# Optimization experiments

Hardware: AMD Instinct MI355X
Metric: run time of the kernel (lower is better)

## Reference

```python
import jax, jax.numpy as jnp
import numpy as np
from jax import lax

NUM_CLASSES = 10
NUM_ITER = 3
DN = ('NCHW', 'OIHW', 'NCHW')


def squash(t, axis=-1):
    sq = (t ** 2).sum(axis=axis, keepdims=True)
    return (sq / (1.0 + sq)) * t / jnp.sqrt(sq)


def setup_inputs() -> dict:
    key = jax.random.key(0)
    ks = jax.random.split(key, 12)
    B = 512
    s = 0.05  # param scale for numerical stability
    return {
        'x': jax.random.normal(ks[0], (B, 1, 28, 28), jnp.float32),
        'conv1_w': jax.random.normal(ks[1], (256, 1, 9, 9), jnp.float32) * s,
        'conv1_b': jax.random.normal(ks[2], (256,), jnp.float32) * s,
        'prim_w': jax.random.normal(ks[3], (8, 32, 256, 9, 9), jnp.float32) * s,
        'prim_b': jax.random.normal(ks[4], (8, 32), jnp.float32) * s,
        'route_w': jax.random.normal(ks[5], (NUM_CLASSES, 32 * 6 * 6, 8, 16), jnp.float32),
        'dec_w1': jax.random.normal(ks[6], (512, 16 * NUM_CLASSES), jnp.float32) * s,
        'dec_b1': jax.random.normal(ks[7], (512,), jnp.float32) * s,
        'dec_w2': jax.random.normal(ks[8], (1024, 512), jnp.float32) * s,
        'dec_b2': jax.random.normal(ks[9], (1024,), jnp.float32) * s,
        'dec_w3': jax.random.normal(ks[10], (784, 1024), jnp.float32) * s,
        'dec_b3': jax.random.normal(ks[11], (784,), jnp.float32) * s,
    }


def reference(x, conv1_w, conv1_b, prim_w, prim_b, route_w,
              dec_w1, dec_b1, dec_w2, dec_b2, dec_w3, dec_b3):
    B = x.shape[0]
    # conv1 + relu: [B,256,20,20]
    h = lax.conv_general_dilated(x, conv1_w, (1, 1), 'VALID', dimension_numbers=DN)
    h = jax.nn.relu(h + conv1_b[None, :, None, None])
    # primary capsules: 8 parallel convs fused into one conv with 8*32 out channels
    kw = prim_w.reshape(8 * 32, 256, 9, 9)
    u = lax.conv_general_dilated(h, kw, (2, 2), 'VALID', dimension_numbers=DN)
    u = u + prim_b.reshape(-1)[None, :, None, None]          # [B,256,6,6]
    u = u.reshape(B, 8, 32 * 6 * 6).transpose(0, 2, 1)       # [B,1152,8]
    u = squash(u, axis=-1)
    # digit capsules: priors [C,B,R,16]
    priors = jnp.einsum('bri,crio->cbro', u, route_w)
    logits = jnp.zeros_like(priors)
    for i in range(NUM_ITER):
        probs = jax.nn.softmax(logits, axis=2)
        v = squash((probs * priors).sum(axis=2, keepdims=True))  # [C,B,1,16]
        if i != NUM_ITER - 1:
            logits = logits + (priors * v).sum(axis=-1, keepdims=True)
    caps = v.squeeze(2).transpose(1, 0, 2)                    # [B,C,16]
    classes = jnp.sqrt((caps ** 2).sum(axis=-1))              # [B,C]
    classes = jax.nn.softmax(classes, axis=1)
    y = jax.nn.one_hot(jnp.argmax(classes, axis=1), NUM_CLASSES, dtype=caps.dtype)
    d = (caps * y[:, :, None]).reshape(B, -1)                 # [B,160]
    d = jax.nn.relu(d @ dec_w1.T + dec_b1)
    d = jax.nn.relu(d @ dec_w2.T + dec_b2)
    recon = jax.nn.sigmoid(d @ dec_w3.T + dec_b3)             # [B,784]
    return classes, recon
```

## Files before the change

kernel.cpp:

```cpp
#include <hip/hip_runtime.h>
#include <math.h>


typedef _Float16 f16;
typedef _Float16 f16x8 __attribute__((ext_vector_type(8)));
typedef _Float16 f16x4 __attribute__((ext_vector_type(4)));
typedef float f32x4 __attribute__((ext_vector_type(4)));

__device__ __forceinline__ void gl_lds16(const void* g, void* l) {
  __builtin_amdgcn_global_load_lds(
      (const __attribute__((address_space(1))) void*)g,
      (__attribute__((address_space(3))) void*)l, 16, 0, 0);
}

__global__ __launch_bounds__(256, 2) void conv1_kernel(
    const float* __restrict__ x, const float* __restrict__ w,
    const float* __restrict__ bias, f16* __restrict__ ht)
{
  __shared__ float xs[784];
  const int b = blockIdx.x;
  const int t = threadIdx.x;
  for (int i = t; i < 784; i += 256) xs[i] = x[b * 784 + i];
  float wr[81];
#pragma unroll
  for (int k = 0; k < 81; ++k) wr[k] = w[t * 81 + k];
  const float bv = bias[t];
  __syncthreads();
  for (int oy = 0; oy < 20; ++oy) {
    float acc[20];
#pragma unroll
    for (int i = 0; i < 20; ++i) acc[i] = bv;
#pragma unroll
    for (int ky = 0; ky < 9; ++ky) {
      float xr[28];
#pragma unroll
      for (int q = 0; q < 7; ++q) {
        const float4 v = *(const float4*)&xs[(oy + ky) * 28 + q * 4];
        xr[q*4+0] = v.x; xr[q*4+1] = v.y; xr[q*4+2] = v.z; xr[q*4+3] = v.w;
      }
#pragma unroll
      for (int kx = 0; kx < 9; ++kx) {
        const float wv = wr[ky * 9 + kx];
#pragma unroll
        for (int ox = 0; ox < 20; ++ox) acc[ox] = fmaf(xr[ox + kx], wv, acc[ox]);
      }
    }
    f16* hp = &ht[(size_t)((b * 20 + oy) * 20) * 256 + t];
#pragma unroll
    for (int ox = 0; ox < 20; ++ox)
      hp[ox * 256] = (f16)fmaxf(acc[ox], 0.f);
  }
}

__global__ __launch_bounds__(256) void wtrans_kernel(
    const float* __restrict__ w, f16* __restrict__ wt)
{
  __shared__ float tile[64 * 83];
  const int oc = blockIdx.x;
  const int icq = blockIdx.y;
  const int t = threadIdx.x;
  const float* src = w + (size_t)oc * 20736 + (size_t)icq * 64 * 81;
  for (int idx = t; idx < 5184; idx += 256) {
    const int ici = idx / 81, kk = idx - ici * 81;
    tile[ici * 83 + kk] = src[idx];
  }
  __syncthreads();
  f16* dst = wt + (size_t)oc * 20736 + icq * 64;
  for (int idx = t; idx < 5184; idx += 256) {
    const int kk = idx >> 6, ici = idx & 63;
    dst[kk * 256 + ici] = (f16)tile[ici * 83 + kk];
  }
}

__global__ __launch_bounds__(256) void prim_mfma_kernel(
    const f16* __restrict__ ht, const f16* __restrict__ wt,
    float* __restrict__ part)
{
  __shared__ f16 sm[10240];
  f16* As = sm;
  f16* Bs = sm + 2048;
  const int t = threadIdx.x;
  const int wv = t >> 6, lane = t & 63;
  const int id = blockIdx.x;
  const int ks = (id & 7) >> 1;
  const int mb = ((id >> 3) << 1) | (id & 1);
  const int m0 = mb * 64;

  const int chunk = (lane & 3) ^ ((lane >> 3) & 3);
  long aoff;
  {
    const int r = wv * 16 + (lane >> 2);
    const int m = m0 + r;
    const int b = m / 36, pos = m - b * 36;
    const int oy = pos / 6, ox = pos - oy * 6;
    aoff = (long)(((b * 20 + 2 * oy) * 20 + 2 * ox) * 256) * 2 + chunk * 16;
  }
  long boff[4];
#pragma unroll
  for (int i = 0; i < 4; ++i) {
    const int r = i * 64 + wv * 16 + (lane >> 2);
    boff[i] = (long)r * 41472 + chunk * 16;
  }
  const char* htc = (const char*)ht;
  const char* wtc = (const char*)wt;

  const int lrow = lane & 15, quad = lane >> 4;
  const int qx = quad ^ ((lrow >> 1) & 3);
  f32x4 acc[4][4] = {};

  const int s0 = ks * 162, s1 = s0 + 162;
  for (int s = s0; s < s1; ++s) {
    const int kykx = s >> 3, icb = s & 7;
    const int ky = kykx / 9, kx = kykx - ky * 9;
    const long astep = (long)((((ky * 20 + kx) * 256) + icb * 32) * 2);
    const long bstep = (long)(((kykx * 256) + icb * 32) * 2);
    __syncthreads();
    {
      gl_lds16(htc + aoff + astep, (char*)As + wv * 1024);
#pragma unroll
      for (int i = 0; i < 4; ++i)
        gl_lds16(wtc + boff[i] + bstep, (char*)Bs + i * 4096 + wv * 1024);
    }
    __syncthreads();
    f16x8 af[4], bf[4];
#pragma unroll
    for (int mt = 0; mt < 4; ++mt)
      af[mt] = *(const f16x8*)&As[(mt * 16 + lrow) * 32 + qx * 8];
#pragma unroll
    for (int nt = 0; nt < 4; ++nt)
      bf[nt] = *(const f16x8*)&Bs[(wv * 64 + nt * 16 + lrow) * 32 + qx * 8];
#pragma unroll
    for (int mt = 0; mt < 4; ++mt)
#pragma unroll
      for (int nt = 0; nt < 4; ++nt)
        acc[mt][nt] = __builtin_amdgcn_mfma_f32_16x16x32_f16(
            af[mt], bf[nt], acc[mt][nt], 0, 0, 0);
  }

  float* pp = part + (size_t)ks * 4718592;
#pragma unroll
  for (int mt = 0; mt < 4; ++mt) {
    const int mbase = m0 + mt * 16 + quad * 4;
#pragma unroll
    for (int nt = 0; nt < 4; ++nt) {
      const int n = wv * 64 + nt * 16 + lrow;
      const int np = (n & 31) * 8 + (n >> 5);
#pragma unroll
      for (int rg = 0; rg < 4; ++rg)
        pp[(size_t)(mbase + rg) * 256 + np] = acc[mt][nt][rg];
    }
  }
}

__global__ void squash_kernel(const float* __restrict__ part,
                              const float* __restrict__ bias,
                              float* __restrict__ u)
{
  const int tid = blockIdx.x * 256 + threadIdx.x;
  if (tid >= 512 * 36 * 32) return;
  const int cc = tid & 31;
  const int row = tid >> 5;
  const int b = row / 36;
  const int pos = row - b * 36;
  const float* p = part + (size_t)row * 256 + cc * 8;
  float v[8] = {};
#pragma unroll
  for (int ksl = 0; ksl < 4; ++ksl) {
    const float4 a0 = *(const float4*)(p + (size_t)ksl * 4718592);
    const float4 a1 = *(const float4*)(p + (size_t)ksl * 4718592 + 4);
    v[0] += a0.x; v[1] += a0.y; v[2] += a0.z; v[3] += a0.w;
    v[4] += a1.x; v[5] += a1.y; v[6] += a1.z; v[7] += a1.w;
  }
  float sq = 0.f;
#pragma unroll
  for (int i = 0; i < 8; ++i) {
    v[i] += bias[i * 32 + cc];
    sq = fmaf(v[i], v[i], sq);
  }
  const float scale = sq / ((1.f + sq) * sqrtf(sq));
  float* up = &u[(size_t)(b * 1152 + cc * 36 + pos) * 8];
#pragma unroll
  for (int i = 0; i < 8; ++i) up[i] = v[i] * scale;
}

__global__ __launch_bounds__(256, 4) void priors_kernel(
    const float* __restrict__ u, const float* __restrict__ rw,
    f16* __restrict__ P)
{
  const int t = threadIdx.x;
  const int rl = t >> 2, oq = t & 3;
  const int r = blockIdx.x * 64 + rl;
  const int b0 = blockIdx.y * 64;
  const int c = blockIdx.z;

  float4 wreg[8];
  const float* wbase = rw + (size_t)(c * 1152 + r) * 128 + oq * 4;
#pragma unroll
  for (int k = 0; k < 8; ++k)
    wreg[k] = *(const float4*)(wbase + k * 16);

  f16* pbase = P + (size_t)((c * 512 + b0) * 1152 + r) * 16 + oq * 4;
  const float* ubase = u + (size_t)(b0 * 1152 + r) * 8;

  for (int b = 0; b < 64; ++b) {
    const float4 ua = *(const float4*)(ubase + (size_t)b * 9216);
    const float4 ub = *(const float4*)(ubase + (size_t)b * 9216 + 4);
    const float uu[8] = {ua.x, ua.y, ua.z, ua.w, ub.x, ub.y, ub.z, ub.w};
    float ax = 0.f, ay = 0.f, az = 0.f, aw = 0.f;
#pragma unroll
    for (int k = 0; k < 8; ++k) {
      ax = fmaf(uu[k], wreg[k].x, ax);
      ay = fmaf(uu[k], wreg[k].y, ay);
      az = fmaf(uu[k], wreg[k].z, az);
      aw = fmaf(uu[k], wreg[k].w, aw);
    }
    f16x4 st;
    st[0] = (f16)ax; st[1] = (f16)ay; st[2] = (f16)az; st[3] = (f16)aw;
    *(f16x4*)(pbase + (size_t)b * 18432) = st;
  }
}

__device__ __forceinline__ float wave_sum(float v) {
#pragma unroll
  for (int off = 32; off > 0; off >>= 1) v += __shfl_xor(v, off);
  return v;
}
__device__ __forceinline__ float wave_max(float v) {
#pragma unroll
  for (int off = 32; off > 0; off >>= 1) v = fmaxf(v, __shfl_xor(v, off));
  return v;
}

__global__ __launch_bounds__(256, 2) void routing_kernel(
    const f16* __restrict__ Pg, float* __restrict__ caps)
{
  const int c = blockIdx.x >> 9;
  const int b = blockIdx.x & 511;
  const int t = threadIdx.x;
  const int wid = t >> 6;
  const int lane = t & 63;
  __shared__ float xred[4 * 17];

  float P[5][16];
  float lg[5];
  const int nk = (t < 128) ? 5 : 4;
#pragma unroll
  for (int k = 0; k < 5; ++k)
#pragma unroll
    for (int o = 0; o < 16; ++o) P[k][o] = 0.f;

  const f16* pbase = Pg + (size_t)((c * 512 + b) * 1152) * 16;
#pragma unroll
  for (int k = 0; k < 5; ++k) {
    if (k < nk) {
      const int r = t + (k << 8);
      const f16x8 p0 = *(const f16x8*)&pbase[(size_t)r * 16];
      const f16x8 p1 = *(const f16x8*)&pbase[(size_t)r * 16 + 8];
#pragma unroll
      for (int o = 0; o < 8; ++o) {
        P[k][o]     = (float)p0[o];
        P[k][o + 8] = (float)p1[o];
      }
    }
  }

  float v[16];
  {
    float sq = 0.f;
#pragma unroll
    for (int o = 0; o < 16; ++o) {
      float p = 0.f;
#pragma unroll
      for (int k = 0; k < 5; ++k) p += P[k][o];
      p = wave_sum(p);
      if (lane == 0) xred[wid * 17 + o] = p;
      v[o] = 0.f;
    }
    __syncthreads();
#pragma unroll
    for (int o = 0; o < 16; ++o) {
      const float s = (xred[o] + xred[17 + o] + xred[34 + o] + xred[51 + o]) *
                      (1.f / 1152.f);
      v[o] = s;
      sq = fmaf(s, s, sq);
    }
    const float scale = sq / ((1.f + sq) * sqrtf(sq));
#pragma unroll
    for (int o = 0; o < 16; ++o) v[o] *= scale;
    __syncthreads();
  }
#pragma unroll
  for (int k = 0; k < 5; ++k) {
    float a = 0.f;
#pragma unroll
    for (int o = 0; o < 16; ++o) a = fmaf(P[k][o], v[o], a);
    lg[k] = a;
  }

  for (int it = 1; it < 3; ++it) {
    float m = -1e30f;
#pragma unroll
    for (int k = 0; k < 5; ++k) if (k < nk) m = fmaxf(m, lg[k]);
    m = wave_max(m);
    if (lane == 0) xred[wid * 17 + 16] = m;
    __syncthreads();
    const float mx = fmaxf(fmaxf(xred[16], xred[17 + 16]),
                           fmaxf(xred[34 + 16], xred[51 + 16]));
    __syncthreads();
    float e[5];
#pragma unroll
    for (int k = 0; k < 5; ++k) e[k] = (k < nk) ? expf(lg[k] - mx) : 0.f;
    float pS = 0.f;
#pragma unroll
    for (int k = 0; k < 5; ++k) pS += e[k];
    pS = wave_sum(pS);
    if (lane == 0) xred[wid * 17 + 16] = pS;
#pragma unroll
    for (int o = 0; o < 16; ++o) {
      float p = 0.f;
#pragma unroll
      for (int k = 0; k < 5; ++k) p = fmaf(e[k], P[k][o], p);
      p = wave_sum(p);
      if (lane == 0) xred[wid * 17 + o] = p;
    }
    __syncthreads();
    const float S = xred[16] + xred[17 + 16] + xred[34 + 16] + xred[51 + 16];
    const float inv = 1.f / S;
    float sq = 0.f;
#pragma unroll
    for (int o = 0; o < 16; ++o) {
      const float s = (xred[o] + xred[17 + o] + xred[34 + o] + xred[51 + o]) * inv;
      v[o] = s;
      sq = fmaf(s, s, sq);
    }
    const float scale = sq / ((1.f + sq) * sqrtf(sq));
#pragma unroll
    for (int o = 0; o < 16; ++o) v[o] *= scale;
    __syncthreads();
    if (it < 2) {
#pragma unroll
      for (int k = 0; k < 5; ++k) {
        float a = 0.f;
#pragma unroll
        for (int o = 0; o < 16; ++o) a = fmaf(P[k][o], v[o], a);
        lg[k] += a;
      }
    }
  }
  if (t == 0) {
    float* cp = &caps[(b * 10 + c) * 16];
#pragma unroll
    for (int o = 0; o < 16; ++o) cp[o] = v[o];
  }
}

__global__ void classes_kernel(const float* __restrict__ caps,
                               float* __restrict__ out_classes,
                               float* __restrict__ d0)
{
  const int b = blockIdx.x * 256 + threadIdx.x;
  if (b >= 512) return;
  float nrm[10];
#pragma unroll
  for (int cc = 0; cc < 10; ++cc) {
    float sq = 0.f;
#pragma unroll
    for (int o = 0; o < 16; ++o) {
      const float vv = caps[(b * 10 + cc) * 16 + o];
      sq = fmaf(vv, vv, sq);
    }
    nrm[cc] = sqrtf(sq);
  }
  float mx = nrm[0]; int cs = 0;
#pragma unroll
  for (int cc = 1; cc < 10; ++cc)
    if (nrm[cc] > mx) { mx = nrm[cc]; cs = cc; }
  float e[10], ssum = 0.f;
#pragma unroll
  for (int cc = 0; cc < 10; ++cc) { e[cc] = expf(nrm[cc] - mx); ssum += e[cc]; }
  const float inv = 1.f / ssum;
#pragma unroll
  for (int cc = 0; cc < 10; ++cc) out_classes[b * 10 + cc] = e[cc] * inv;
#pragma unroll
  for (int cc = 0; cc < 10; ++cc)
#pragma unroll
    for (int o = 0; o < 16; ++o)
      d0[b * 160 + cc * 16 + o] = (cc == cs) ? caps[(b * 10 + cc) * 16 + o] : 0.f;
}

__global__ __launch_bounds__(256, 2) void fc_kernel(
    const float* __restrict__ A, const float* __restrict__ W,
    const float* __restrict__ bias, float* __restrict__ C,
    int N, int K, int act)
{
  __shared__ float As[64][17];
  __shared__ float Ws[64][17];
  const int t = threadIdx.x;
  const int tm = t >> 4, tn = t & 15;
  const int m0 = blockIdx.y << 6, n0 = blockIdx.x << 6;
  const int lr = t >> 2, lq = (t & 3) << 2;
  float acc[4][4] = {};
  for (int k0 = 0; k0 < K; k0 += 16) {
    const float4 av = *(const float4*)&A[(m0 + lr) * K + k0 + lq];
    float4 wv = make_float4(0.f, 0.f, 0.f, 0.f);
    const int wn = n0 + lr;
    if (wn < N) wv = *(const float4*)&W[wn * K + k0 + lq];
    __syncthreads();
    As[lr][lq+0] = av.x; As[lr][lq+1] = av.y; As[lr][lq+2] = av.z; As[lr][lq+3] = av.w;
    Ws[lr][lq+0] = wv.x; Ws[lr][lq+1] = wv.y; Ws[lr][lq+2] = wv.z; Ws[lr][lq+3] = wv.w;
    __syncthreads();
#pragma unroll
    for (int kk = 0; kk < 16; ++kk) {
      float a[4], w[4];
#pragma unroll
      for (int i = 0; i < 4; ++i) a[i] = As[tm * 4 + i][kk];
#pragma unroll
      for (int j = 0; j < 4; ++j) w[j] = Ws[tn * 4 + j][kk];
#pragma unroll
      for (int i = 0; i < 4; ++i)
#pragma unroll
        for (int j = 0; j < 4; ++j) acc[i][j] = fmaf(a[i], w[j], acc[i][j]);
    }
  }
#pragma unroll
  for (int i = 0; i < 4; ++i) {
    const int m = m0 + tm * 4 + i;
#pragma unroll
    for (int j = 0; j < 4; ++j) {
      const int n = n0 + tn * 4 + j;
      if (n < N) {
        float vv = acc[i][j] + bias[n];
        vv = act ? (1.f / (1.f + expf(-vv))) : fmaxf(vv, 0.f);
        C[m * N + n] = vv;
      }
    }
  }
}

extern "C" void kernel_launch(void* const* d_in, const int* in_sizes, int n_in,
                              void* d_out, int out_size, void* d_ws, size_t ws_size,
                              hipStream_t stream)
{
  const float* x       = (const float*)d_in[0];
  const float* conv1_w = (const float*)d_in[1];
  const float* conv1_b = (const float*)d_in[2];
  const float* prim_w  = (const float*)d_in[3];
  const float* prim_b  = (const float*)d_in[4];
  const float* route_w = (const float*)d_in[5];
  const float* dec_w1  = (const float*)d_in[6];
  const float* dec_b1  = (const float*)d_in[7];
  const float* dec_w2  = (const float*)d_in[8];
  const float* dec_b2  = (const float*)d_in[9];
  const float* dec_w3  = (const float*)d_in[10];
  const float* dec_b3  = (const float*)d_in[11];
  float* out = (float*)d_out;

  char* ws = (char*)d_ws;
  f16*   ht   = (f16*)(ws);
  f16*   wtp  = (f16*)(ws + 104857600);
  float* part = (float*)(ws + 115474432);
  float* u    = (float*)(ws + 190971904);
  f16*   P    = (f16*)(ws);
  float* caps = (float*)(ws + 209846272);
  float* d0   = (float*)(ws + 210173952);
  float* d1   = (float*)(ws + 210501632);
  float* d2   = (float*)(ws + 211550208);

  hipLaunchKernelGGL(conv1_kernel, dim3(512), dim3(256), 0, stream,
                     x, conv1_w, conv1_b, ht);
  hipLaunchKernelGGL(wtrans_kernel, dim3(256, 4), dim3(256), 0, stream,
                     prim_w, wtp);
  hipLaunchKernelGGL(prim_mfma_kernel, dim3(1152), dim3(256), 0, stream,
                     ht, wtp, part);
  hipLaunchKernelGGL(squash_kernel, dim3(2304), dim3(256), 0, stream,
                     part, prim_b, u);
  hipLaunchKernelGGL(priors_kernel, dim3(18, 8, 10), dim3(256), 0, stream,
                     u, route_w, P);
  hipLaunchKernelGGL(routing_kernel, dim3(5120), dim3(256), 0, stream,
                     P, caps);
  hipLaunchKernelGGL(classes_kernel, dim3(2), dim3(256), 0, stream,
                     caps, out, d0);
  hipLaunchKernelGGL(fc_kernel, dim3(8, 8), dim3(256), 0, stream,
                     d0, dec_w1, dec_b1, d1, 512, 160, 0);
  hipLaunchKernelGGL(fc_kernel, dim3(16, 8), dim3(256), 0, stream,
                     d1, dec_w2, dec_b2, d2, 1024, 512, 0);
  hipLaunchKernelGGL(fc_kernel, dim3(13, 8), dim3(256), 0, stream,
                     d2, dec_w3, dec_b3, out + 5120, 784, 1024, 1);
}
```

Before: 857.3 us.

## Retile primary-capsule MFMA GEMM to 128x128 blocks with 64-wide K steps

Changes the primary-capsule conv GEMM block tile from 64x256 with K=32 per step to 128x128 with K=64 per step, using a 2x2 wave layout and an 8-chunk XOR swizzle in LDS. Each barrier pair now covers two MFMA rounds, halving the number of K iterations and synchronisation points. The square tile balances global loads between A and B. LDS use grows to 32KB per block and the grid mapping is reorganised across M, N and K-split.

After: 841.5 us. About the same (-1.8%).

```diff
diff --git a/kernel.cpp b/kernel.cpp
--- a/kernel.cpp
+++ b/kernel.cpp
@@ -76,74 +76,80 @@
     const f16* __restrict__ ht, const f16* __restrict__ wt,
     float* __restrict__ part)
 {
-  __shared__ f16 sm[10240];
-  f16* As = sm;
-  f16* Bs = sm + 2048;
+  __shared__ f16 sm[16384];
   const int t = threadIdx.x;
   const int wv = t >> 6, lane = t & 63;
   const int id = blockIdx.x;
-  const int ks = (id & 7) >> 1;
-  const int mb = ((id >> 3) << 1) | (id & 1);
-  const int m0 = mb * 64;
-
-  const int chunk = (lane & 3) ^ ((lane >> 3) & 3);
-  long aoff;
-  {
-    const int r = wv * 16 + (lane >> 2);
+  const int g = id >> 3;
+  const int ks = g & 3;
+  const int nb = (g >> 2) & 1;
+  const int mb = (id & 7) + 8 * (g >> 3);
+  const int m0 = mb * 128, n0 = nb * 128;
+
+  const int chunk = (lane & 7) ^ ((lane >> 3) & 7);
+  long aoff[4], boff[4];
+#pragma unroll
+  for (int i = 0; i < 4; ++i) {
+    const int r = wv * 32 + i * 8 + (lane >> 3);
     const int m = m0 + r;
     const int b = m / 36, pos = m - b * 36;
     const int oy = pos / 6, ox = pos - oy * 6;
-    aoff = (long)(((b * 20 + 2 * oy) * 20 + 2 * ox) * 256) * 2 + chunk * 16;
-  }
-  long boff[4];
-#pragma unroll
-  for (int i = 0; i < 4; ++i) {
-    const int r = i * 64 + wv * 16 + (lane >> 2);
-    boff[i] = (long)r * 41472 + chunk * 16;
+    aoff[i] = (long)(((b * 20 + 2 * oy) * 20 + 2 * ox) * 256) * 2 + chunk * 16;
+    boff[i] = (long)(n0 + r) * 41472 + chunk * 16;
   }
   const char* htc = (const char*)ht;
   const char* wtc = (const char*)wt;
 
   const int lrow = lane & 15, quad = lane >> 4;
-  const int qx = quad ^ ((lrow >> 1) & 3);
+  const int wm = wv & 1, wn = wv >> 1;
   f32x4 acc[4][4] = {};
 
-  const int s0 = ks * 162, s1 = s0 + 162;
+  const int s0 = ks * 81, s1 = s0 + 81;
   for (int s = s0; s < s1; ++s) {
-    const int kykx = s >> 3, icb = s & 7;
+    const int kykx = s >> 2, icb = s & 3;
     const int ky = kykx / 9, kx = kykx - ky * 9;
-    const long astep = (long)((((ky * 20 + kx) * 256) + icb * 32) * 2);
-    const long bstep = (long)(((kykx * 256) + icb * 32) * 2);
+    const long astep = (long)((((ky * 20 + kx) * 256) + icb * 64) * 2);
+    const long bstep = (long)(((kykx * 256) + icb * 64) * 2);
     __syncthreads();
     {
-      gl_lds16(htc + aoff + astep, (char*)As + wv * 1024);
-#pragma unroll
-      for (int i = 0; i < 4; ++i)
-        gl_lds16(wtc + boff[i] + bstep, (char*)Bs + i * 4096 + wv * 1024);
-    }
-    __syncthreads();
-    f16x8 af[4], bf[4];
-#pragma unroll
-    for (int mt = 0; mt < 4; ++mt)
-      af[mt] = *(const f16x8*)&As[(mt * 16 + lrow) * 32 + qx * 8];
-#pragma unroll
-    for (int nt = 0; nt < 4; ++nt)
-      bf[nt] = *(const f16x8*)&Bs[(wv * 64 + nt * 16 + lrow) * 32 + qx * 8];
-#pragma unroll
-    for (int mt = 0; mt < 4; ++mt)
+      char* dA = (char*)sm + wv * 4096;
+      char* dB = (char*)sm + 16384 + wv * 4096;
+#pragma unroll
+      for (int i = 0; i < 4; ++i) {
+        gl_lds16(htc + aoff[i] + astep, dA + i * 1024);
+        gl_lds16(wtc + boff[i] + bstep, dB + i * 1024);
+      }
+    }
+    __syncthreads();
+    const f16* As = sm;
+    const f16* Bs = sm + 8192;
+#pragma unroll
+    for (int h = 0; h < 2; ++h) {
+      f16x8 af[4], bf[4];
+      const int cbase = h * 4 + quad;
+      const int cp = cbase ^ (lrow & 7);
+#pragma unroll
+      for (int mt = 0; mt < 4; ++mt)
+        af[mt] = *(const f16x8*)&As[(wm * 64 + mt * 16 + lrow) * 64 + cp * 8];
 #pragma unroll
       for (int nt = 0; nt < 4; ++nt)
-        acc[mt][nt] = __builtin_amdgcn_mfma_f32_16x16x32_f16(
-            af[mt], bf[nt], acc[mt][nt], 0, 0, 0);
+        bf[nt] = *(const f16x8*)&Bs[(wn * 64 + nt * 16 + lrow) * 64 + cp * 8];
+#pragma unroll
+      for (int mt = 0; mt < 4; ++mt)
+#pragma unroll
+        for (int nt = 0; nt < 4; ++nt)
+          acc[mt][nt] = __builtin_amdgcn_mfma_f32_16x16x32_f16(
+              af[mt], bf[nt], acc[mt][nt], 0, 0, 0);
+    }
   }
 
   float* pp = part + (size_t)ks * 4718592;
 #pragma unroll
   for (int mt = 0; mt < 4; ++mt) {
-    const int mbase = m0 + mt * 16 + quad * 4;
+    const int mbase = m0 + wm * 64 + mt * 16 + quad * 4;
 #pragma unroll
     for (int nt = 0; nt < 4; ++nt) {
-      const int n = wv * 64 + nt * 16 + lrow;
+      const int n = n0 + wn * 64 + nt * 16 + lrow;
       const int np = (n & 31) * 8 + (n >> 5);
 #pragma unroll
       for (int rg = 0; rg < 4; ++rg)
```
